# Optimization experiments

Hardware: AMD Instinct MI355X
Metric: run time of the kernel (lower is better)

## Reference

```python
import jax, jax.numpy as jnp
import numpy as np

D_MODEL = 1024
NUM_EXPERTS = 16
TOP_K = 2
TOP_C = 4  # min(E, max(4, 2*top_k))
TAU = 1.0
RANK = 64  # max(4, d_model // 16)


def _stable_softmax(v):
    m = jnp.max(v, axis=-1, keepdims=True)
    e = jnp.exp(v - m)
    return e / (jnp.sum(e, axis=-1, keepdims=True) + 1e-12)


def setup_inputs() -> dict:
    key = jax.random.key(0)
    ks = jax.random.split(key, 8)
    B, D, E, R = 16384, D_MODEL, NUM_EXPERTS, RANK
    x = jax.random.normal(ks[0], (B, D), dtype=jnp.float32)
    W_enc = jax.random.normal(ks[1], (D, D), dtype=jnp.float32) * (1.0 / np.sqrt(D))
    b_enc = jnp.zeros((D,), dtype=jnp.float32)
    W_gate = jax.random.normal(ks[2], (E, D), dtype=jnp.float32) * (1.0 / np.sqrt(D))
    U = jax.random.normal(ks[3], (E, R, D), dtype=jnp.float32) * (1.0 / np.sqrt(D))
    V = jax.random.normal(ks[4], (E, D, R), dtype=jnp.float32) * (1.0 / np.sqrt(R))
    gamma = jnp.ones((E,), dtype=jnp.float32)
    return {"x": x, "W_enc": W_enc, "b_enc": b_enc, "W_gate": W_gate,
            "U": U, "V": V, "gamma": gamma}


def reference(x, W_enc, b_enc, W_gate, U, V, gamma):
    # shared encoder
    encoded = x @ W_enc.T + b_enc                      # [B, D]
    # gating: logits -> top_c -> top_k -> softmax over selected logits
    logits = (encoded @ W_gate.T) / TAU                # [B, E]
    topc_vals, topc_idx = jax.lax.top_k(logits, TOP_C)
    topk_vals, pos_in_c = jax.lax.top_k(topc_vals, TOP_K)
    topk_idx = jnp.take_along_axis(topc_idx, pos_in_c, axis=1)  # [B, K]
    topk_w = _stable_softmax(topk_vals)                # [B, K], all > 1e-12
    # dense per-(token, expert) combine weight (equivalent to gather/scatter)
    B = x.shape[0]
    w_dense = jnp.zeros((B, NUM_EXPERTS), dtype=x.dtype)
    w_dense = w_dense.at[jnp.arange(B)[:, None], topk_idx].add(topk_w)
    # low-rank experts: delta_e(x) = gamma_e * silu(x U_e^T) V_e^T
    s = jax.nn.silu(jnp.einsum('bd,erd->ber', encoded, U))        # [B, E, R]
    coef = w_dense * gamma[None, :]                               # [B, E]
    delta = jnp.einsum('ber,edr->bd', s * coef[..., None], V)     # [B, D]
    # y = encoded + sum_k w_k * (expert(x) - x)  with expert(x)-x = delta_e
    return encoded + delta
```

## Files before the change

kernel.cpp:

```cpp
#include <hip/hip_runtime.h>
#include <hip/hip_bf16.h>

#define D_DIM 1024
#define NE 16
#define RK 64
#define NTOK 16384

typedef __bf16 bf16;
typedef __bf16 bf16x8 __attribute__((ext_vector_type(8)));
typedef __bf16 bf16x4 __attribute__((ext_vector_type(4)));
typedef float f32x4 __attribute__((ext_vector_type(4)));

__device__ __forceinline__ void gload16(const void* g, void* l) {
  __builtin_amdgcn_global_load_lds((const __attribute__((address_space(1))) unsigned int*)g,
                                   (__attribute__((address_space(3))) unsigned int*)l,
                                   16, 0, 0);
}

__global__ void k_cast(const float* __restrict__ s, bf16* __restrict__ d, int n4) {
  int i = blockIdx.x * blockDim.x + threadIdx.x;
  if (i >= n4) return;
  float4 v = ((const float4*)s)[i];
  bf16x4 o = { (bf16)v.x, (bf16)v.y, (bf16)v.z, (bf16)v.w };
  ((bf16x4*)d)[i] = o;
}

__global__ void k_castv(const float* __restrict__ V, bf16* __restrict__ Vb2) {
  int id = blockIdx.x * 256 + threadIdx.x;
  int d = id & 1023;
  int rb = (id >> 10) & 7;
  int e = id >> 13;
  const float* src = V + ((size_t)(e * 1024 + d)) * 64 + rb * 8;
  float4 v0 = *(const float4*)src;
  float4 v1 = *(const float4*)(src + 4);
  bf16x8 o = { (bf16)v0.x, (bf16)v0.y, (bf16)v0.z, (bf16)v0.w,
               (bf16)v1.x, (bf16)v1.y, (bf16)v1.z, (bf16)v1.w };
  *(bf16x8*)(Vb2 + (size_t)id * 8) = o;
}

__global__ void k_gmat(const float* __restrict__ Wg, const float* __restrict__ We,
                       float* __restrict__ Gt2) {
  int d = blockIdx.x * 256 + threadIdx.x;
  int e = blockIdx.y;
  int j0 = blockIdx.z * 128;
  double a0 = 0.0, a1 = 0.0, a2 = 0.0, a3 = 0.0;
  for (int j = j0; j < j0 + 128; j += 4) {
    a0 += (double)Wg[e * D_DIM + j + 0] * (double)We[(size_t)(j + 0) * D_DIM + d];
    a1 += (double)Wg[e * D_DIM + j + 1] * (double)We[(size_t)(j + 1) * D_DIM + d];
    a2 += (double)Wg[e * D_DIM + j + 2] * (double)We[(size_t)(j + 2) * D_DIM + d];
    a3 += (double)Wg[e * D_DIM + j + 3] * (double)We[(size_t)(j + 3) * D_DIM + d];
  }
  atomicAdd(&Gt2[(d >> 2) * 64 + e * 4 + (d & 3)], (float)((a0 + a1) + (a2 + a3)));
}

__global__ void k_bgate(const float* __restrict__ Wg, const float* __restrict__ be,
                        float* __restrict__ bg) {
  __shared__ double red[256];
  int e = blockIdx.x, t = threadIdx.x;
  double a = 0.0;
  for (int j = t; j < D_DIM; j += 256) a += (double)Wg[e * D_DIM + j] * (double)be[j];
  red[t] = a; __syncthreads();
  for (int s = 128; s > 0; s >>= 1) { if (t < s) red[t] += red[t + s]; __syncthreads(); }
  if (t == 0) bg[e] = (float)red[0];
}

__global__ __launch_bounds__(256) void k_gatecast(const float* __restrict__ x,
                                                  const float* __restrict__ Gt2,
                                                  const float* __restrict__ bg,
                                                  const float* __restrict__ gamma,
                                                  bf16* __restrict__ xb,
                                                  int* __restrict__ pk,
                                                  float2* __restrict__ wpair) {
  __shared__ float bufx[8][1024];
  __shared__ float Ls[4 * 2 * NE];
  int tid = threadIdx.x;
  int wv = tid >> 6, lane = tid & 63;
  int g = lane & 15;
  int s = lane >> 4;
  int tokbase = blockIdx.x * 8 + wv * 2;

  const float* xr0 = x + (size_t)tokbase * D_DIM;
#pragma unroll
  for (int c = 0; c < 4; ++c) {
    gload16(xr0 + c * 256 + lane * 4, &bufx[wv * 2][c * 256 + lane * 4]);
    gload16(xr0 + D_DIM + c * 256 + lane * 4, &bufx[wv * 2 + 1][c * 256 + lane * 4]);
  }

  const float* Gq = Gt2 + s * 64 + g * 4;
  const float* b0p = &bufx[wv * 2][s * 4];
  const float* b1p = &bufx[wv * 2 + 1][s * 4];
  float acc0 = 0.0f, acc1 = 0.0f;
  float4 ga = *(const float4*)(Gq + 0 * 256);
  float4 gb = *(const float4*)(Gq + 1 * 256);
  float4 gc = *(const float4*)(Gq + 2 * 256);
  float4 gd = *(const float4*)(Gq + 3 * 256);
  for (int c = 0; c < 16; ++c) {
    int base = c * 4;
    int nb = (c < 15) ? base + 4 : base;
    float4 na = *(const float4*)(Gq + (size_t)(nb + 0) * 256);
    float4 nb4 = *(const float4*)(Gq + (size_t)(nb + 1) * 256);
    float4 nc = *(const float4*)(Gq + (size_t)(nb + 2) * 256);
    float4 nd = *(const float4*)(Gq + (size_t)(nb + 3) * 256);
#define GSTEP(GV, J)                                                        \
    {                                                                       \
      float4 x0 = *(const float4*)(b0p + (base + (J)) * 16);                \
      float4 x1 = *(const float4*)(b1p + (base + (J)) * 16);                \
      acc0 += x0.x * GV.x + x0.y * GV.y + x0.z * GV.z + x0.w * GV.w;        \
      acc1 += x1.x * GV.x + x1.y * GV.y + x1.z * GV.z + x1.w * GV.w;        \
    }
    GSTEP(ga, 0) GSTEP(gb, 1) GSTEP(gc, 2) GSTEP(gd, 3)
#undef GSTEP
    ga = na; gb = nb4; gc = nc; gd = nd;
  }
  acc0 += __shfl_xor(acc0, 16); acc0 += __shfl_xor(acc0, 32);
  acc1 += __shfl_xor(acc1, 16); acc1 += __shfl_xor(acc1, 32);
  if (s == 0) {
    Ls[wv * 32 + g] = acc0;
    Ls[wv * 32 + 16 + g] = acc1;
  }

#pragma unroll
  for (int t = 0; t < 2; ++t) {
    const float4* src = (const float4*)&bufx[wv * 2 + t][0];
    bf16x4* dst = (bf16x4*)(xb + (size_t)(tokbase + t) * D_DIM);
#pragma unroll
    for (int r = 0; r < 4; ++r) {
      float4 v = src[lane + 64 * r];
      bf16x4 o = { (bf16)v.x, (bf16)v.y, (bf16)v.z, (bf16)v.w };
      dst[lane + 64 * r] = o;
    }
  }
  __syncthreads();

  if (lane < 2) {
    int t = lane;
    int tok = tokbase + t;
    const float* lrow = &Ls[wv * 32 + t * 16];
    float v1 = -1e30f, v2 = -1e30f; int i1 = 0, i2 = 0;
#pragma unroll
    for (int e = 0; e < NE; ++e) {
      float v = lrow[e] + bg[e];
      if (v > v1) { v2 = v1; i2 = i1; v1 = v; i1 = e; }
      else if (v > v2) { v2 = v; i2 = e; }
    }
    float e1 = expf(v2 - v1);
    float den = 1.0f + e1 + 1e-12f;
    float w0 = (1.0f / den) * gamma[i1];
    float w1 = (e1 / den) * gamma[i2];
    pk[tok] = i1 | (i2 << 8);
    wpair[tok] = make_float2(w0, w1);
  }
}

__global__ __launch_bounds__(256) void k_scatter(const int* __restrict__ pk,
                                                 const float2* __restrict__ wpair,
                                                 int* __restrict__ cnt,
                                                 int* __restrict__ lists,
                                                 float* __restrict__ wl) {
  __shared__ int lc[32];
  __shared__ int base[32];
  __shared__ int lc2[32];
  int tid = threadIdx.x;
  int tok = blockIdx.x * 256 + tid;
  if (tid < 32) { lc[tid] = 0; lc2[tid] = 0; }
  __syncthreads();
  int p = pk[tok];
  float2 w = wpair[tok];
  int b0 = p & 0xff;
  int b1 = 16 + ((p >> 8) & 0xff);
  atomicAdd(&lc[b0], 1);
  atomicAdd(&lc[b1], 1);
  __syncthreads();
  if (tid < 32 && lc[tid] > 0) base[tid] = atomicAdd(&cnt[tid], lc[tid]);
  __syncthreads();
  int r0 = base[b0] + atomicAdd(&lc2[b0], 1);
  lists[(size_t)b0 * NTOK + r0] = tok;
  wl[(size_t)b0 * NTOK + r0] = w.x;
  int r1 = base[b1] + atomicAdd(&lc2[b1], 1);
  lists[(size_t)b1 * NTOK + r1] = tok;
  wl[(size_t)b1 * NTOK + r1] = w.y;
}

__global__ void k_btab(const int* __restrict__ cnt, int2* __restrict__ btab,
                       int* __restrict__ nblk) {
  int lane = threadIdx.x;
  int nb = (lane < 32) ? ((cnt[lane] + 63) >> 6) : 0;
  int pfx = nb;
  for (int off = 1; off < 32; off <<= 1) {
    int v = __shfl_up(pfx, off);
    if (lane >= off) pfx += v;
  }
  int start = pfx - nb;
  if (lane < 32) {
    int c = cnt[lane];
    int i = 0;
    for (int t0 = 0; t0 < c; t0 += 64, ++i)
      btab[start + i] = make_int2(lane, t0);
  }
  if (lane == 31) *nblk = pfx;
}

__global__ __launch_bounds__(512, 1) void k_encgemm(const bf16* __restrict__ A,
                                                    const bf16* __restrict__ W,
                                                    const float* __restrict__ bias,
                                                    bf16* __restrict__ encb) {
  __shared__ char smem[65536];
  bf16* const AsB = (bf16*)smem;
  bf16* const BsB = (bf16*)(smem + 32768);
  int tid = threadIdx.x;
  int w = blockIdx.x;
  int bm = (w & 63) * 256;
  int bn = (w >> 6) * 256;
  int lane = tid & 63, wv = tid >> 6;
  int wm = (wv >> 2) * 128, wn = (wv & 3) * 64;
  int srow = tid >> 2;
  int sc = (tid & 3) * 8;
  int fr = lane & 15, fk = (lane >> 4) * 8;
  f32x4 acc[8][4] = {};

  {
    bf16* as = AsB; bf16* bs = BsB;
    gload16(A + (size_t)(bm + srow) * D_DIM + sc, &as[srow * 32 + sc]);
    gload16(A + (size_t)(bm + 128 + srow) * D_DIM + sc, &as[(128 + srow) * 32 + sc]);
    gload16(W + (size_t)(bn + srow) * D_DIM + sc, &bs[srow * 32 + sc]);
    gload16(W + (size_t)(bn + 128 + srow) * D_DIM + sc, &bs[(128 + srow) * 32 + sc]);
  }
  __syncthreads();

  for (int k0 = 0; k0 < D_DIM; k0 += 32) {
    int cur = (k0 >> 5) & 1;
    if (k0 + 32 < D_DIM) {
      int kn = k0 + 32;
      bf16* as = AsB + (cur ^ 1) * 8192;
      bf16* bs = BsB + (cur ^ 1) * 8192;
      gload16(A + (size_t)(bm + srow) * D_DIM + kn + sc, &as[srow * 32 + sc]);
      gload16(A + (size_t)(bm + 128 + srow) * D_DIM + kn + sc, &as[(128 + srow) * 32 + sc]);
      gload16(W + (size_t)(bn + srow) * D_DIM + kn + sc, &bs[srow * 32 + sc]);
      gload16(W + (size_t)(bn + 128 + srow) * D_DIM + kn + sc, &bs[(128 + srow) * 32 + sc]);
    }
    const bf16* as = AsB + cur * 8192;
    const bf16* bs = BsB + cur * 8192;
    bf16x8 af[8], bv[4];
#pragma unroll
    for (int m = 0; m < 8; ++m)
      af[m] = *(const bf16x8*)&as[(wm + m * 16 + fr) * 32 + fk];
#pragma unroll
    for (int n = 0; n < 4; ++n)
      bv[n] = *(const bf16x8*)&bs[(wn + n * 16 + fr) * 32 + fk];
    __builtin_amdgcn_s_setprio(1);
#pragma unroll
    for (int m = 0; m < 8; ++m)
#pragma unroll
      for (int n = 0; n < 4; ++n)
        acc[m][n] = __builtin_amdgcn_mfma_f32_16x16x32_bf16(af[m], bv[n], acc[m][n], 0, 0, 0);
    __builtin_amdgcn_s_setprio(0);
    __syncthreads();
  }

  int rg = (lane >> 4) * 4;
  bf16* tb = (bf16*)smem + wv * 2176;
#pragma unroll
  for (int h = 0; h < 4; ++h) {
#pragma unroll
    for (int mi = 0; mi < 2; ++mi) {
      int m = h * 2 + mi;
#pragma unroll
      for (int n = 0; n < 4; ++n) {
        float bval = bias[bn + wn + n * 16 + fr];
#pragma unroll
        for (int r = 0; r < 4; ++r)
          tb[(mi * 16 + rg + r) * 68 + n * 16 + fr] = (bf16)(acc[m][n][r] + bval);
      }
    }
#pragma unroll
    for (int it2 = 0; it2 < 8; ++it2) {
      int row = it2 * 4 + (lane >> 4);
      int c4 = (lane & 15) * 4;
      *(ushort4*)&encb[(size_t)(bm + wm + h * 32 + row) * D_DIM + bn + wn + c4] =
        *(const ushort4*)&tb[row * 68 + c4];
    }
  }
}

__global__ __launch_bounds__(256) void k_expert(const bf16* __restrict__ encb,
                                                const bf16* __restrict__ Ub,
                                                const bf16* __restrict__ Vb2,
                                                const int* __restrict__ cnt,
                                                const int* __restrict__ lists,
                                                const float* __restrict__ wl,
                                                const int2* __restrict__ btab,
                                                const int* __restrict__ nblk,
                                                bf16* __restrict__ d0,
                                                bf16* __restrict__ d1) {
  int bid = blockIdx.x;
  if (bid >= *nblk) return;
  int2 bt = btab[bid];
  int bin = bt.x, t0 = bt.y;
  int slot = bin >> 4, e = bin & 15;
  int c = cnt[bin];
  int nrows = c - t0; if (nrows > 64) nrows = 64;
  const int* tl = lists + (size_t)bin * NTOK + t0;
  const float* wlp = wl + (size_t)bin * NTOK + t0;

  __shared__ int toks[64];
  __shared__ float coefs[64];
  __shared__ bf16 AU[8192];
  __shared__ bf16 Ss[64 * 64];
  bf16* const As = AU;
  bf16* const Us = AU + 4096;

  int tid = threadIdx.x;
  if (tid < 64) {
    int rr = tid < nrows ? tid : nrows - 1;
    toks[tid] = tl[rr];
    coefs[tid] = tid < nrows ? wlp[tid] : 0.0f;
  }
  __syncthreads();

  int lane = tid & 63, wv = tid >> 6;
  int srow = tid >> 3;
  int sc8 = tid & 7;
  int scol = sc8 * 8;
  int cs = (sc8 ^ (srow & 7)) * 8;
  int fr = lane & 15, fk = (lane >> 4) * 8;
  int sw = (fr & 7) << 3;
  size_t tokA0 = (size_t)toks[srow] * D_DIM;
  size_t tokA1 = (size_t)toks[32 + srow] * D_DIM;
  const bf16* Ue = Ub + (size_t)e * RK * D_DIM;
  f32x4 acc1[4] = {};

  for (int k0 = 0; k0 < D_DIM; k0 += 64) {
    __syncthreads();
    gload16(encb + tokA0 + k0 + cs, &As[srow * 64 + scol]);
    gload16(encb + tokA1 + k0 + cs, &As[(32 + srow) * 64 + scol]);
    gload16(Ue + (size_t)srow * D_DIM + k0 + cs, &Us[srow * 64 + scol]);
    gload16(Ue + (size_t)(32 + srow) * D_DIM + k0 + cs, &Us[(32 + srow) * 64 + scol]);
    __syncthreads();
    __builtin_amdgcn_s_setprio(1);
#pragma unroll
    for (int kk = 0; kk < 2; ++kk) {
      bf16x8 af = *(const bf16x8*)&As[((wv * 16 + fr) * 64 + kk * 32 + fk) ^ sw];
#pragma unroll
      for (int n = 0; n < 4; ++n) {
        bf16x8 bv = *(const bf16x8*)&Us[((n * 16 + fr) * 64 + kk * 32 + fk) ^ sw];
        acc1[n] = __builtin_amdgcn_mfma_f32_16x16x32_bf16(af, bv, acc1[n], 0, 0, 0);
      }
    }
    __builtin_amdgcn_s_setprio(0);
  }
  int rg = (lane >> 4) * 4;
#pragma unroll
  for (int n = 0; n < 4; ++n)
#pragma unroll
    for (int r = 0; r < 4; ++r) {
      int row = wv * 16 + rg + r;
      float v = acc1[n][r];
      float s = v / (1.0f + __expf(-v));
      Ss[(row * 64 + n * 16 + fr) ^ (((rg + r) & 7) << 3)] = (bf16)(s * coefs[row]);
    }
  __syncthreads();
  bf16x8 a2[4][2];
#pragma unroll
  for (int m = 0; m < 4; ++m)
#pragma unroll
    for (int kk = 0; kk < 2; ++kk)
      a2[m][kk] = *(const bf16x8*)&Ss[((m * 16 + fr) * 64 + kk * 32 + fk) ^ sw];
  __syncthreads();

  const bf16* Ve2 = Vb2 + (size_t)e * RK * D_DIM;
  bf16* dst = slot ? d1 : d0;
  int rb0 = lane >> 4;
  int colbase = wv * 256;
  bf16* tb = AU + wv * 2048;
  for (int njb = 0; njb < 8; ++njb) {
#pragma unroll
    for (int nj2 = 0; nj2 < 2; ++nj2) {
      int nj = njb * 2 + nj2;
      int dcol = colbase + nj * 16 + fr;
      bf16x8 b0 = *(const bf16x8*)&Ve2[((size_t)rb0 * D_DIM + dcol) * 8];
      bf16x8 b1 = *(const bf16x8*)&Ve2[((size_t)(rb0 + 4) * D_DIM + dcol) * 8];
#pragma unroll
      for (int m = 0; m < 4; ++m) {
        f32x4 a = {};
        a = __builtin_amdgcn_mfma_f32_16x16x32_bf16(a2[m][0], b0, a, 0, 0, 0);
        a = __builtin_amdgcn_mfma_f32_16x16x32_bf16(a2[m][1], b1, a, 0, 0, 0);
#pragma unroll
        for (int r = 0; r < 4; ++r)
          tb[(m * 16 + rg + r) * 32 + nj2 * 16 + fr] = (bf16)a[r];
      }
    }
#pragma unroll
    for (int it2 = 0; it2 < 16; ++it2) {
      int row = it2 * 4 + (lane >> 4);
      int c2 = (lane & 15) * 2;
      if (row < nrows)
        *(ushort2*)&dst[(size_t)toks[row] * D_DIM + colbase + njb * 32 + c2] =
          *(const ushort2*)&tb[row * 32 + c2];
    }
  }
}

__global__ __launch_bounds__(256) void k_final(float* __restrict__ out,
                                               const bf16* __restrict__ encb,
                                               const bf16* __restrict__ d0,
                                               const bf16* __restrict__ d1) {
  size_t i = ((size_t)blockIdx.x * 256 + threadIdx.x) * 8;
  bf16x8 e = *(const bf16x8*)(encb + i);
  bf16x8 a = *(const bf16x8*)(d0 + i);
  bf16x8 b = *(const bf16x8*)(d1 + i);
  float4 o0, o1;
  o0.x = (float)e[0] + (float)a[0] + (float)b[0];
  o0.y = (float)e[1] + (float)a[1] + (float)b[1];
  o0.z = (float)e[2] + (float)a[2] + (float)b[2];
  o0.w = (float)e[3] + (float)a[3] + (float)b[3];
  o1.x = (float)e[4] + (float)a[4] + (float)b[4];
  o1.y = (float)e[5] + (float)a[5] + (float)b[5];
  o1.z = (float)e[6] + (float)a[6] + (float)b[6];
  o1.w = (float)e[7] + (float)a[7] + (float)b[7];
  *(float4*)(out + i) = o0;
  *(float4*)(out + i + 4) = o1;
}

extern "C" void kernel_launch(void* const* d_in, const int* in_sizes, int n_in,
                              void* d_out, int out_size, void* d_ws, size_t ws_size,
                              hipStream_t stream) {
  const float* x   = (const float*)d_in[0];
  const float* We  = (const float*)d_in[1];
  const float* be  = (const float*)d_in[2];
  const float* Wg  = (const float*)d_in[3];
  const float* U   = (const float*)d_in[4];
  const float* V   = (const float*)d_in[5];
  const float* gam = (const float*)d_in[6];
  float* out = (float*)d_out;
  char* ws = (char*)d_ws;

  int*    cnt  = (int*)(ws + 0);
  float*  Gt2  = (float*)(ws + 256);
  float*  bg   = (float*)(ws + 66048);
  int2*   btab = (int2*)(ws + 66176);
  int*    nblk = (int*)(ws + 70656);
  bf16*   xb   = (bf16*)(ws + 131072);
  bf16*   d0   = (bf16*)(ws + 131072);
  bf16*   encb = (bf16*)(ws + 131072 + 33554432);
  char*   base = ws + 131072 + 2 * 33554432;
  bf16*   Wb   = (bf16*)(base);
  bf16*   Ubf  = (bf16*)(base + 2097152);
  bf16*   Vb2  = (bf16*)(base + 2 * 2097152);
  int*    lists= (int*)(base + 3 * 2097152);
  float*  wl   = (float*)(base + 4 * 2097152);
  int*    pk   = (int*)(base + 5 * 2097152);
  float2* wpr  = (float2*)(base + 5 * 2097152 + 131072);
  bf16*   d1   = (bf16*)(base + 5 * 2097152 + 131072 + 131072 + 131072);

  hipMemsetAsync(ws, 0, 66048, stream);

  k_cast<<<1024, 256, 0, stream>>>(We, Wb, 1048576 / 4);
  k_cast<<<1024, 256, 0, stream>>>(U, Ubf, 1048576 / 4);
  k_castv<<<512, 256, 0, stream>>>(V, Vb2);

  dim3 gg(4, 16, 8);
  k_gmat<<<gg, 256, 0, stream>>>(Wg, We, Gt2);
  k_bgate<<<16, 256, 0, stream>>>(Wg, be, bg);

  k_gatecast<<<2048, 256, 0, stream>>>(x, Gt2, bg, gam, xb, pk, wpr);
  k_scatter<<<64, 256, 0, stream>>>(pk, wpr, cnt, lists, wl);
  k_btab<<<1, 64, 0, stream>>>(cnt, btab, nblk);

  k_encgemm<<<256, 512, 0, stream>>>(xb, Wb, be, encb);

  k_expert<<<544, 256, 0, stream>>>(encb, Ubf, Vb2, cnt, lists, wl, btab, nblk, d0, d1);
  k_final<<<8192, 256, 0, stream>>>(out, encb, d0, d1);
}
```

Before: 161.1 us.

## Double K-tile depth to 64 with XOR-swizzled LDS layout in encoder GEMM

```diff
diff --git a/kernel.cpp b/kernel.cpp
--- a/kernel.cpp
+++ b/kernel.cpp
@@ -204,61 +204,70 @@
                                                     const bf16* __restrict__ W,
                                                     const float* __restrict__ bias,
                                                     bf16* __restrict__ encb) {
-  __shared__ char smem[65536];
-  bf16* const AsB = (bf16*)smem;
-  bf16* const BsB = (bf16*)(smem + 32768);
+  __shared__ bf16 AsB[2 * 256 * 64];
+  __shared__ bf16 BsB[2 * 256 * 64];
   int tid = threadIdx.x;
   int w = blockIdx.x;
   int bm = (w & 63) * 256;
   int bn = (w >> 6) * 256;
   int lane = tid & 63, wv = tid >> 6;
   int wm = (wv >> 2) * 128, wn = (wv & 3) * 64;
-  int srow = tid >> 2;
-  int sc = (tid & 3) * 8;
+  int srow = tid >> 3;
+  int sc8 = tid & 7;
+  int scol = sc8 * 8;
+  int cs = (sc8 ^ (srow & 7)) * 8;
   int fr = lane & 15, fk = (lane >> 4) * 8;
   f32x4 acc[8][4] = {};
 
-  {
-    bf16* as = AsB; bf16* bs = BsB;
-    gload16(A + (size_t)(bm + srow) * D_DIM + sc, &as[srow * 32 + sc]);
-    gload16(A + (size_t)(bm + 128 + srow) * D_DIM + sc, &as[(128 + srow) * 32 + sc]);
-    gload16(W + (size_t)(bn + srow) * D_DIM + sc, &bs[srow * 32 + sc]);
-    gload16(W + (size_t)(bn + 128 + srow) * D_DIM + sc, &bs[(128 + srow) * 32 + sc]);
-  }
-  __syncthreads();
-
-  for (int k0 = 0; k0 < D_DIM; k0 += 32) {
-    int cur = (k0 >> 5) & 1;
-    if (k0 + 32 < D_DIM) {
-      int kn = k0 + 32;
-      bf16* as = AsB + (cur ^ 1) * 8192;
-      bf16* bs = BsB + (cur ^ 1) * 8192;
-      gload16(A + (size_t)(bm + srow) * D_DIM + kn + sc, &as[srow * 32 + sc]);
-      gload16(A + (size_t)(bm + 128 + srow) * D_DIM + kn + sc, &as[(128 + srow) * 32 + sc]);
-      gload16(W + (size_t)(bn + srow) * D_DIM + kn + sc, &bs[srow * 32 + sc]);
-      gload16(W + (size_t)(bn + 128 + srow) * D_DIM + kn + sc, &bs[(128 + srow) * 32 + sc]);
-    }
-    const bf16* as = AsB + cur * 8192;
-    const bf16* bs = BsB + cur * 8192;
-    bf16x8 af[8], bv[4];
-#pragma unroll
-    for (int m = 0; m < 8; ++m)
-      af[m] = *(const bf16x8*)&as[(wm + m * 16 + fr) * 32 + fk];
-#pragma unroll
-    for (int n = 0; n < 4; ++n)
-      bv[n] = *(const bf16x8*)&bs[(wn + n * 16 + fr) * 32 + fk];
+#pragma unroll
+  for (int p = 0; p < 4; ++p) {
+    int r = p * 64 + srow;
+    gload16(A + (size_t)(bm + r) * D_DIM + cs, &AsB[r * 64 + scol]);
+    gload16(W + (size_t)(bn + r) * D_DIM + cs, &BsB[r * 64 + scol]);
+  }
+  __syncthreads();
+
+  for (int k0 = 0; k0 < D_DIM; k0 += 64) {
+    int cur = (k0 >> 6) & 1;
+    if (k0 + 64 < D_DIM) {
+      int kn = k0 + 64;
+      bf16* as = AsB + (cur ^ 1) * 16384;
+      bf16* bs = BsB + (cur ^ 1) * 16384;
+#pragma unroll
+      for (int p = 0; p < 4; ++p) {
+        int r = p * 64 + srow;
+        gload16(A + (size_t)(bm + r) * D_DIM + kn + cs, &as[r * 64 + scol]);
+        gload16(W + (size_t)(bn + r) * D_DIM + kn + cs, &bs[r * 64 + scol]);
+      }
+    }
+    const bf16* as = AsB + cur * 16384;
+    const bf16* bs = BsB + cur * 16384;
     __builtin_amdgcn_s_setprio(1);
 #pragma unroll
-    for (int m = 0; m < 8; ++m)
-#pragma unroll
-      for (int n = 0; n < 4; ++n)
-        acc[m][n] = __builtin_amdgcn_mfma_f32_16x16x32_bf16(af[m], bv[n], acc[m][n], 0, 0, 0);
+    for (int kk = 0; kk < 2; ++kk) {
+      bf16x8 af[8], bv[4];
+#pragma unroll
+      for (int m = 0; m < 8; ++m) {
+        int row = wm + m * 16 + fr;
+        af[m] = *(const bf16x8*)&as[(row * 64 + kk * 32 + fk) ^ ((row & 7) << 3)];
+      }
+#pragma unroll
+      for (int n = 0; n < 4; ++n) {
+        int row = wn + n * 16 + fr;
+        bv[n] = *(const bf16x8*)&bs[(row * 64 + kk * 32 + fk) ^ ((row & 7) << 3)];
+      }
+#pragma unroll
+      for (int m = 0; m < 8; ++m)
+#pragma unroll
+        for (int n = 0; n < 4; ++n)
+          acc[m][n] = __builtin_amdgcn_mfma_f32_16x16x32_bf16(af[m], bv[n], acc[m][n], 0, 0, 0);
+    }
     __builtin_amdgcn_s_setprio(0);
     __syncthreads();
   }
 
   int rg = (lane >> 4) * 4;
-  bf16* tb = (bf16*)smem + wv * 2176;
+  bf16* tb = AsB + wv * 2176;
 #pragma unroll
   for (int h = 0; h < 4; ++h) {
 #pragma unroll
```

After: 163.3 us. No clear change (+1.4%).
